# Performance work log

Hardware: AMD Instinct MI355X
Metric: run time of the kernel (lower is better)

Reference implementation:

```python
import jax, jax.numpy as jnp
import numpy as np

B, K, BIN = 16, 2048, 256
GRU, EMB, HID = 1024, 1024, 1024
H, KV = 16, 4
D = HID // H          # 64 head dim
NREP = H // KV        # 4 GQA repeat factor


def rotate_half(x):
    x1, x2 = jnp.split(x, 2, axis=-1)
    return jnp.concatenate((-x2, x1), axis=-1)


def setup_inputs() -> dict:
    key = jax.random.key(0)
    ks = jax.random.split(key, 8)
    h = jax.random.normal(ks[0], (B, K, GRU), dtype=jnp.float32)
    # real RoPE frequency tables, shape (BIN, D)
    inv_freq = 1.0 / (10000.0 ** (jnp.arange(0, D, 2, dtype=jnp.float32) / D))
    t = jnp.arange(BIN, dtype=jnp.float32)
    freqs = jnp.outer(t, inv_freq)                      # (BIN, D/2)
    emb = jnp.concatenate((freqs, freqs), axis=-1)      # (BIN, D)
    freqs_cos, freqs_sin = jnp.cos(emb), jnp.sin(emb)
    s = lambda fan: 1.0 / np.sqrt(fan).astype(np.float32)
    Wq = jax.random.normal(ks[1], (H * D, EMB), jnp.float32) * s(EMB)
    Wk = jax.random.normal(ks[2], (KV * D, GRU), jnp.float32) * s(GRU)
    Wv = jax.random.normal(ks[3], (KV * D, GRU), jnp.float32) * s(GRU)
    Wo = jax.random.normal(ks[4], (EMB, H * D), jnp.float32) * s(H * D)
    output_queries = jax.random.normal(ks[5], (BIN, EMB), jnp.float32)
    Wr = jax.random.normal(ks[6], (2, EMB), jnp.float32) * s(EMB)
    br = jnp.zeros((2,), jnp.float32)
    return {"h": h, "freqs_cos": freqs_cos, "freqs_sin": freqs_sin,
            "Wq": Wq, "Wk": Wk, "Wv": Wv, "Wo": Wo,
            "output_queries": output_queries, "Wr": Wr, "br": br}


def reference(h, freqs_cos, freqs_sin, Wq, Wk, Wv, Wo, output_queries, Wr, br):
    # KV projections from GRU history: (B, K, KV, D)
    k = (h @ Wk.T).reshape(B, K, KV, D)
    v = (h @ Wv.T).reshape(B, K, KV, D)
    # Queries are batch-invariant learned tokens: (BIN, H, D)
    q = (output_queries @ Wq.T).reshape(BIN, H, D)
    cos = freqs_cos[:, None, :]  # (BIN, 1, D) broadcast over heads
    sin = freqs_sin[:, None, :]
    q = q * cos + rotate_half(q) * sin
    # GQA: repeat_interleave KV heads to H heads
    k_rep = jnp.repeat(k, NREP, axis=2)  # (B, K, H, D)
    v_rep = jnp.repeat(v, NREP, axis=2)
    scores = jnp.einsum('qhd,bkhd->bhqk', q, k_rep) / np.sqrt(D).astype(np.float32)
    attn = jax.nn.softmax(scores, axis=-1)               # dropout p=0 (eval)
    out = jnp.einsum('bhqk,bkhd->bqhd', attn, v_rep).reshape(B, BIN, H * D)
    z = out @ Wo.T                                        # (B, BIN, EMB)
    return z @ Wr.T + br                                  # (B, BIN, 2)
```

## Files before the change

### kernel.cpp

```cpp
#include <hip/hip_runtime.h>

typedef __attribute__((ext_vector_type(8))) short short8;
typedef __attribute__((ext_vector_type(4))) float f32x4;
typedef __attribute__((ext_vector_type(16))) float f32x16;

#define DEV static __device__ __forceinline__

DEV unsigned short f2bf(float f) {
  unsigned int u = __float_as_uint(f);
  u += 0x7fff + ((u >> 16) & 1);
  return (unsigned short)(u >> 16);
}

DEV unsigned int cvtpk(float lo, float hi) {
  unsigned int r;
  asm("v_cvt_pk_bf16_f32 %0, %1, %2" : "=v"(r) : "v"(lo), "v"(hi));
  return r;
}

DEV f32x4 mfma16(short8 a, short8 b, f32x4 c) {
  return __builtin_amdgcn_mfma_f32_16x16x32_bf16(a, b, c, 0, 0, 0);
}

DEV f32x16 mfma32(short8 a, short8 b, f32x16 c) {
  return __builtin_amdgcn_mfma_f32_32x32x16_bf16(a, b, c, 0, 0, 0);
}

DEV void gl_lds16(const void* g, void* l) {
  __builtin_amdgcn_global_load_lds((const __attribute__((address_space(1))) void*)g,
                                   (__attribute__((address_space(3))) void*)l, 16, 0, 0);
}

__global__ __launch_bounds__(256) void cvtB_kernel(const float* __restrict__ Wq,
                                                   const float* __restrict__ Wk,
                                                   const float* __restrict__ Wv,
                                                   unsigned short* __restrict__ wqb,
                                                   unsigned short* __restrict__ wkvb) {
  int id = blockIdx.x * 256 + threadIdx.x;
  int e = id * 4;
  float4 v;
  unsigned short* d;
  if (e < 1048576)      { v = *(const float4*)(Wq + e);             d = wqb + e; }
  else if (e < 1310720) { v = *(const float4*)(Wk + (e - 1048576)); d = wkvb + (e - 1048576); }
  else                  { v = *(const float4*)(Wv + (e - 1310720)); d = wkvb + 262144 + (e - 1310720); }
  uint2 pk;
  pk.x = cvtpk(v.x, v.y);
  pk.y = cvtpk(v.z, v.w);
  *(uint2*)d = pk;
}

__global__ __launch_bounds__(256) void wrp_partial(const float* __restrict__ Wr,
                                                   const float* __restrict__ Wo,
                                                   float* __restrict__ part) {
  int blk = blockIdx.x;
  int tid = threadIdx.x;
  float a0[4] = {0.f,0.f,0.f,0.f};
  float a1[4] = {0.f,0.f,0.f,0.f};
  int e0 = blk * 64;
  for (int e = e0; e < e0 + 64; e++) {
    float w0 = Wr[e];
    float w1 = Wr[1024 + e];
    #pragma unroll
    for (int j4 = 0; j4 < 4; j4++) {
      float wo = Wo[(size_t)e * 1024 + j4 * 256 + tid];
      a0[j4] += w0 * wo;
      a1[j4] += w1 * wo;
    }
  }
  #pragma unroll
  for (int j4 = 0; j4 < 4; j4++) {
    part[blk * 2048 + 0    + j4 * 256 + tid] = a0[j4];
    part[blk * 2048 + 1024 + j4 * 256 + tid] = a1[j4];
  }
}

__global__ __launch_bounds__(256) void wrp_reduce(const float* __restrict__ part,
                                                  float* __restrict__ Wrp) {
  int id = blockIdx.x * 256 + threadIdx.x;
  float s = 0.f;
  #pragma unroll
  for (int blk = 0; blk < 16; blk++) s += part[blk * 2048 + id];
  Wrp[id] = s;
}

__global__ __launch_bounds__(512, 2) void gemm_kv(const float* __restrict__ A,
                                                  const unsigned short* __restrict__ Bb,
                                                  unsigned short* __restrict__ ok,
                                                  unsigned short* __restrict__ ov) {
  __shared__ float Asl[3][4096];
  __shared__ unsigned short Bsl[3][16384];

  int bid = blockIdx.x;
  int sw = (bid & 7) * 32 + (bid >> 3);
  int m0 = sw * 128;

  int tid = threadIdx.x;
  int w = tid >> 6, l = tid & 63;
  int l4 = l >> 4, l15 = l & 15;

  int ra = tid >> 3, ua = tid & 7;
  const float* gaA  = A + (size_t)(m0 + ra) * 1024 + ((ua ^ (ra & 7)) * 4);
  const float* gaA2 = gaA + (size_t)64 * 1024;
  const unsigned short* gbB = Bb + (size_t)(tid >> 2) * 1024
                                 + (((tid & 3) ^ ((tid >> 3) & 3)) * 8);

  int aoff0 = l15 * 128 + (((l4 * 2)     ^ (l15 & 7)) * 16);
  int aoff1 = l15 * 128 + (((l4 * 2 + 1) ^ (l15 & 7)) * 16);
  int boff = (w * 64 + l15) * 64 + ((l4 ^ ((l15 >> 1) & 3)) * 16);

  f32x4 acc[8][4];
  #pragma unroll
  for (int i = 0; i < 8; i++)
    #pragma unroll
    for (int j = 0; j < 4; j++) acc[i][j] = (f32x4)(0.f);

  #define STAGE(T, SB)                                                      \
    { const float* a0p = gaA  + (T) * 32;                                   \
      const float* a1p = gaA2 + (T) * 32;                                   \
      gl_lds16(a0p, (char*)Asl[SB] + tid * 16);                             \
      gl_lds16(a1p, (char*)Asl[SB] + 8192 + tid * 16);                      \
      const unsigned short* b0p = gbB + (T) * 32;                           \
      gl_lds16(b0p,          (char*)Bsl[SB] + tid * 16);                    \
      gl_lds16(b0p + 131072, (char*)Bsl[SB] + 8192  + tid * 16);            \
      gl_lds16(b0p + 262144, (char*)Bsl[SB] + 16384 + tid * 16);            \
      gl_lds16(b0p + 393216, (char*)Bsl[SB] + 24576 + tid * 16); }

  #define COMPUTE(CB)                                                       \
    { const char* Ab = (const char*)Asl[CB];                                \
      const char* Bf = (const char*)Bsl[CB];                                \
      short8 bfr[4];                                                        \
      _Pragma("unroll")                                                     \
      for (int j = 0; j < 4; j++)                                           \
        bfr[j] = *(const short8*)(Bf + boff + j * 1024);                    \
      _Pragma("unroll")                                                     \
      for (int i = 0; i < 8; i++) {                                         \
        float4 x = *(const float4*)(Ab + aoff0 + i * 2048);                 \
        float4 y = *(const float4*)(Ab + aoff1 + i * 2048);                 \
        union { short8 s; unsigned int u[4]; } af;                          \
        af.u[0] = cvtpk(x.x, x.y); af.u[1] = cvtpk(x.z, x.w);               \
        af.u[2] = cvtpk(y.x, y.y); af.u[3] = cvtpk(y.z, y.w);               \
        _Pragma("unroll")                                                   \
        for (int j = 0; j < 4; j++)                                         \
          acc[i][j] = mfma16(af.s, bfr[j], acc[i][j]);                      \
      } }

  #define WAIT6                                                             \
    { asm volatile("s_waitcnt vmcnt(6)" ::: "memory");                      \
      __builtin_amdgcn_s_barrier();                                         \
      __builtin_amdgcn_sched_barrier(0); }

  #define WAIT0                                                             \
    { asm volatile("s_waitcnt vmcnt(0)" ::: "memory");                      \
      __builtin_amdgcn_s_barrier();                                         \
      __builtin_amdgcn_sched_barrier(0); }

  STAGE(0, 0);
  STAGE(1, 1);
  asm volatile("s_waitcnt vmcnt(6)" ::: "memory");
  __builtin_amdgcn_s_barrier();
  __builtin_amdgcn_sched_barrier(0);

  #pragma unroll 1
  for (int tb = 0; tb < 30; tb += 3) {
    STAGE(tb + 2, 2); COMPUTE(0); WAIT6;
    STAGE(tb + 3, 0); COMPUTE(1); WAIT6;
    STAGE(tb + 4, 1); COMPUTE(2); WAIT6;
  }
  COMPUTE(0);
  WAIT0;
  COMPUTE(1);

  #undef STAGE
  #undef COMPUTE
  #undef WAIT6
  #undef WAIT0

  #pragma unroll
  for (int i = 0; i < 8; i++)
    #pragma unroll
    for (int j = 0; j < 4; j++) {
      int n = w * 64 + j * 16 + l15;
      int kvv = n >> 6, d = n & 63;
      #pragma unroll
      for (int r = 0; r < 4; r++) {
        int m = m0 + i * 16 + l4 * 4 + r;
        int bb = m >> 11, kk = m & 2047;
        unsigned short val = f2bf(acc[i][j][r]);
        if (kvv < 4)
          ok[((size_t)(bb * 4 + kvv) * 2048 + kk) * 64 + d] = val;
        else
          ov[((size_t)(bb * 4 + (kvv - 4)) * 64 + d) * 2048 + kk] = val;
      }
    }
}

__global__ __launch_bounds__(256) void gemm_q(const float* __restrict__ A,
                                              const unsigned short* __restrict__ Bb,
                                              float* __restrict__ of) {
  __shared__ unsigned short Asm[2][4096];
  __shared__ unsigned short Bsm[2][4096];

  int bid = blockIdx.x;
  int ksplit = bid >> 4;
  int m0 = ((bid >> 3) & 1) * 128;
  int n0 = (bid & 7) * 128;
  int t0 = ksplit * 8;
  constexpr int nt = 8;

  int tid = threadIdx.x;
  int w = tid >> 6, l = tid & 63;
  int l4 = l >> 4, l15 = l & 15;
  int wm = w >> 1, wn = w & 1;

  int ra = w * 32 + (l >> 1);
  int rx = (l >> 2) & 3;
  const float* ga = A + (size_t)(m0 + ra) * 1024 + t0 * 32 + (l & 1) * 16;
  int pw0 = (2 * (l & 1) + 0) ^ rx;
  int pw1 = (2 * (l & 1) + 1) ^ rx;
  int awb0 = ra * 64 + pw0 * 16;
  int awb1 = ra * 64 + pw1 * 16;

  int rb = w * 32 + (l >> 2);
  int cb = ((l & 3) ^ ((l >> 3) & 3)) * 8;
  const unsigned short* gb = Bb + (size_t)(n0 + rb) * 1024 + t0 * 32 + cb;

  int qsw = l4 ^ ((l15 >> 1) & 3);
  int arb = (wm * 64 + l15) * 64 + qsw * 16;
  int brb = (wn * 64 + l15) * 64 + qsw * 16;

  f32x4 acc[4][4];
  #pragma unroll
  for (int i = 0; i < 4; i++)
    #pragma unroll
    for (int j = 0; j < 4; j++) acc[i][j] = (f32x4)(0.f);

  float4 fa0, fa1, fa2, fa3;

  #define LOADA(tt)                                                        \
    { const float* gA = ga + (tt) * 32;                                    \
      fa0 = *(const float4*)(gA);                                          \
      fa1 = *(const float4*)(gA + 4);                                      \
      fa2 = *(const float4*)(gA + 8);                                      \
      fa3 = *(const float4*)(gA + 12); }

  #define WRITEA(bufi)                                                     \
    { union { short8 s; unsigned int u[4]; } t0u, t1u;                     \
      t0u.u[0] = cvtpk(fa0.x, fa0.y); t0u.u[1] = cvtpk(fa0.z, fa0.w);      \
      t0u.u[2] = cvtpk(fa1.x, fa1.y); t0u.u[3] = cvtpk(fa1.z, fa1.w);      \
      t1u.u[0] = cvtpk(fa2.x, fa2.y); t1u.u[1] = cvtpk(fa2.z, fa2.w);      \
      t1u.u[2] = cvtpk(fa3.x, fa3.y); t1u.u[3] = cvtpk(fa3.z, fa3.w);      \
      *(short8*)((char*)Asm[bufi] + awb0) = t0u.s;                         \
      *(short8*)((char*)Asm[bufi] + awb1) = t1u.s; }

  #define STAGEB(bufi, tt)                                                 \
    { char* lb = (char*)Bsm[bufi] + w * 2048;                              \
      const unsigned short* gB = gb + (tt) * 32;                           \
      gl_lds16(gB, lb);                                                    \
      gl_lds16(gB + 16384, lb + 1024); }

  LOADA(0);
  STAGEB(0, 0);
  WRITEA(0);
  __syncthreads();

  for (int t = 0; t < nt; t++) {
    int buf = t & 1;
    if (t + 1 < nt) {
      LOADA(t + 1);
      STAGEB(buf ^ 1, t + 1);
    }
    short8 af[4], bfg[4];
    #pragma unroll
    for (int i = 0; i < 4; i++)
      af[i] = *(const short8*)((char*)Asm[buf] + arb + i * 1024);
    #pragma unroll
    for (int j = 0; j < 4; j++)
      bfg[j] = *(const short8*)((char*)Bsm[buf] + brb + j * 1024);
    #pragma unroll
    for (int i = 0; i < 4; i++)
      #pragma unroll
      for (int j = 0; j < 4; j++)
        acc[i][j] = mfma16(af[i], bfg[j], acc[i][j]);
    if (t + 1 < nt) WRITEA(buf ^ 1);
    __syncthreads();
  }
  #undef LOADA
  #undef WRITEA
  #undef STAGEB

  float* o = of + (size_t)ksplit * 262144;
  #pragma unroll
  for (int i = 0; i < 4; i++)
    #pragma unroll
    for (int j = 0; j < 4; j++) {
      int n = n0 + wn * 64 + j * 16 + l15;
      #pragma unroll
      for (int r = 0; r < 4; r++) {
        int m = m0 + wm * 64 + i * 16 + l4 * 4 + r;
        o[(size_t)m * 1024 + n] = acc[i][j][r];
      }
    }
}

__global__ __launch_bounds__(256) void rope_kernel(const float* __restrict__ qp,
                                                   const float* __restrict__ cosb,
                                                   const float* __restrict__ sinb,
                                                   unsigned short* __restrict__ qb) {
  int id = blockIdx.x * 256 + threadIdx.x;
  int qrow = id >> 10, hd = id & 1023, hh = hd >> 6, d = hd & 63;
  int od = hh * 64 + ((d < 32) ? d + 32 : d - 32);
  float v = 0.f, o = 0.f;
  #pragma unroll
  for (int s4 = 0; s4 < 4; s4++) {
    v += qp[s4 * 262144 + qrow * 1024 + hd];
    o += qp[s4 * 262144 + qrow * 1024 + od];
  }
  if (d < 32) o = -o;
  float c = cosb[qrow * 64 + d];
  float s = sinb[qrow * 64 + d];
  float outv = (v * c + o * s) * 0.18033688011112042f;
  qb[((size_t)hh * 256 + qrow) * 64 + d] = f2bf(outv);
}

__global__ __launch_bounds__(256) void attn_kernel(const unsigned short* __restrict__ qb,
                                                   const unsigned short* __restrict__ kb,
                                                   const unsigned short* __restrict__ vb,
                                                   const float* __restrict__ Wrp,
                                                   float* __restrict__ part) {
  __shared__ unsigned short Kt[2][2048];
  __shared__ unsigned short Vt[2][2048];

  int bid = blockIdx.x;
  int x = bid & 7, mid = (bid >> 3) & 7, top = bid >> 6;
  int g = mid * 8 + x;
  int b = g >> 2, kvh = g & 3;
  int hl = top >> 1, qh = top & 1;
  int h = kvh * 4 + hl;

  int tid = threadIdx.x;
  int w = tid >> 6, l = tid & 63;
  int q31 = l & 31, L = l >> 5;
  int qg = qh * 128 + w * 32 + q31;

  const unsigned short* kg = kb + (size_t)(b * 4 + kvh) * 2048 * 64;
  const unsigned short* vg = vb + (size_t)(b * 4 + kvh) * 64 * 2048;

  short8 qf[4];
  #pragma unroll
  for (int c = 0; c < 4; c++)
    qf[c] = *(const short8*)&qb[((size_t)h * 256 + qg) * 64 + c * 16 + L * 8];

  f32x16 Ot[2];
  Ot[0] = (f32x16)(0.f); Ot[1] = (f32x16)(0.f);
  float m = -1e30f, lsum = 0.f;

  int ksrow = tid >> 3, kslot = tid & 7;
  const unsigned short* ksrc = kg + (size_t)ksrow * 64 + ((kslot ^ (ksrow & 7)) * 8);
  int vsrow = tid >> 2, vslot = tid & 3;
  const unsigned short* vsrc = vg + (size_t)vsrow * 2048 + ((vslot ^ (vsrow & 3)) * 8);

  #define STAGE(bufi, tt)                                                    \
    { gl_lds16(ksrc + (size_t)(tt) * 2048, (char*)Kt[bufi] + tid * 16);      \
      gl_lds16(vsrc + (tt) * 32,           (char*)Vt[bufi] + tid * 16); }

  STAGE(0, 0);
  __syncthreads();

  for (int t = 0; t < 64; t++) {
    int buf = t & 1;
    if (t + 1 < 64) STAGE(buf ^ 1, t + 1);

    f32x16 st = (f32x16)(0.f);
    #pragma unroll
    for (int c = 0; c < 4; c++) {
      int row = q31;
      int byt = row * 128 + (((c * 2 + L) ^ (row & 7)) * 16);
      short8 kf = *(const short8*)((char*)Kt[buf] + byt);
      st = mfma32(kf, qf[c], st);
    }

    float mx = fmaxf(fmaxf(fmaxf(st[0], st[1]), fmaxf(st[2], st[3])),
                     fmaxf(fmaxf(st[4], st[5]), fmaxf(st[6], st[7])));
    float mx2 = fmaxf(fmaxf(fmaxf(st[8], st[9]), fmaxf(st[10], st[11])),
                      fmaxf(fmaxf(st[12], st[13]), fmaxf(st[14], st[15])));
    mx = fmaxf(mx, mx2);
    mx = fmaxf(mx, __shfl_xor(mx, 32));

    if (!__all(mx <= m + 8.f)) {
      float mnew = fmaxf(m, mx);
      float corr = exp2f(m - mnew);
      lsum *= corr;
      #pragma unroll
      for (int db = 0; db < 2; db++)
        #pragma unroll
        for (int r = 0; r < 16; r++) Ot[db][r] *= corr;
      m = mnew;
    }

    float p[16];
    float ls = 0.f;
    #pragma unroll
    for (int r = 0; r < 16; r++) {
      p[r] = exp2f(st[r] - m);
      ls += p[r];
    }
    lsum += ls;

    unsigned int pw[2][4];
    #pragma unroll
    for (int kc = 0; kc < 2; kc++) {
      unsigned int A0 = cvtpk(p[kc * 8 + 0], p[kc * 8 + 1]);
      unsigned int A1 = cvtpk(p[kc * 8 + 2], p[kc * 8 + 3]);
      unsigned int B0 = cvtpk(p[kc * 8 + 4], p[kc * 8 + 5]);
      unsigned int B1 = cvtpk(p[kc * 8 + 6], p[kc * 8 + 7]);
      asm volatile("v_permlane32_swap_b32 %0, %1" : "+v"(A0), "+v"(B0));
      asm volatile("v_permlane32_swap_b32 %0, %1" : "+v"(A1), "+v"(B1));
      pw[kc][0] = A0; pw[kc][1] = A1; pw[kc][2] = B0; pw[kc][3] = B1;
    }

    #pragma unroll
    for (int db = 0; db < 2; db++) {
      int drow = db * 32 + q31;
      #pragma unroll
      for (int kc = 0; kc < 2; kc++) {
        int byt = drow * 64 + (((kc * 2 + L) ^ (drow & 3)) * 16);
        short8 vf = *(const short8*)((char*)Vt[buf] + byt);
        short8 pf;
        {
          union { short8 s; unsigned int u[4]; } uu;
          uu.u[0] = pw[kc][0]; uu.u[1] = pw[kc][1];
          uu.u[2] = pw[kc][2]; uu.u[3] = pw[kc][3];
          pf = uu.s;
        }
        Ot[db] = mfma32(vf, pf, Ot[db]);
      }
    }

    __syncthreads();
  }
  #undef STAGE

  lsum += __shfl_xor(lsum, 32);
  float rinv = 1.0f / lsum;

  float a0 = 0.f, a1 = 0.f;
  #pragma unroll
  for (int db = 0; db < 2; db++)
    #pragma unroll
    for (int rq = 0; rq < 4; rq++) {
      int dbase = db * 32 + rq * 8 + L * 4;
      float4 w0v = *(const float4*)(Wrp + h * 64 + dbase);
      float4 w1v = *(const float4*)(Wrp + 1024 + h * 64 + dbase);
      #pragma unroll
      for (int j = 0; j < 4; j++) {
        float o = Ot[db][rq * 4 + j] * rinv;
        a0 += o * ((const float*)&w0v)[j];
        a1 += o * ((const float*)&w1v)[j];
      }
    }
  a0 += __shfl_xor(a0, 32);
  a1 += __shfl_xor(a1, 32);

  if (L == 0) {
    size_t base = ((size_t)(b * 16 + h) * 256 + qg) * 2;
    float2 r2; r2.x = a0; r2.y = a1;
    *(float2*)&part[base] = r2;
  }
}

__global__ __launch_bounds__(256) void final_kernel(const float* __restrict__ part,
                                                    const float* __restrict__ br,
                                                    float* __restrict__ out) {
  int id = blockIdx.x * 256 + threadIdx.x;
  int c = id & 1, q = (id >> 1) & 255, b = id >> 9;
  float s = br[c];
  #pragma unroll
  for (int hh = 0; hh < 16; hh++)
    s += part[(((size_t)(b * 16 + hh) * 256) + q) * 2 + c];
  out[id] = s;
}

extern "C" void kernel_launch(void* const* d_in, const int* in_sizes, int n_in,
                              void* d_out, int out_size, void* d_ws, size_t ws_size,
                              hipStream_t stream) {
  const float* h    = (const float*)d_in[0];
  const float* fcos = (const float*)d_in[1];
  const float* fsin = (const float*)d_in[2];
  const float* Wq   = (const float*)d_in[3];
  const float* Wk   = (const float*)d_in[4];
  const float* Wv   = (const float*)d_in[5];
  const float* Wo   = (const float*)d_in[6];
  const float* oq   = (const float*)d_in[7];
  const float* Wr   = (const float*)d_in[8];
  const float* br   = (const float*)d_in[9];
  float* out = (float*)d_out;

  char* ws = (char*)d_ws;
  unsigned short* kbuf = (unsigned short*)(ws);
  unsigned short* vbuf = (unsigned short*)(ws + 16777216);
  float* qpart         = (float*)(ws + 33554432);
  unsigned short* qbf  = (unsigned short*)(ws + 37748736);
  float* wpart         = (float*)(ws + 38273024);
  float* Wrp           = (float*)(ws + 38404096);
  float* apart         = (float*)(ws + 38412288);
  unsigned short* wqb  = (unsigned short*)(ws + 38936576);
  unsigned short* wkvb = (unsigned short*)(ws + 41033728);

  cvtB_kernel<<<dim3(1536), dim3(256), 0, stream>>>(Wq, Wk, Wv, wqb, wkvb);
  wrp_partial<<<dim3(16), dim3(256), 0, stream>>>(Wr, Wo, wpart);
  wrp_reduce<<<dim3(8), dim3(256), 0, stream>>>(wpart, Wrp);
  gemm_q<<<dim3(64), dim3(256), 0, stream>>>(oq, wqb, qpart);
  rope_kernel<<<dim3(1024), dim3(256), 0, stream>>>(qpart, fcos, fsin, qbf);
  gemm_kv<<<dim3(256), dim3(512), 0, stream>>>(h, wkvb, kbuf, vbuf);
  attn_kernel<<<dim3(512), dim3(256), 0, stream>>>(qbf, kbuf, vbuf, Wrp, apart);
  final_kernel<<<dim3(32), dim3(256), 0, stream>>>(apart, br, out);
}
```

Measured before the change: 167.8 us.

## Split attention over KV halves and pre-convert A tiles to bf16 in GEMM

```diff
diff --git a/kernel.cpp b/kernel.cpp
--- a/kernel.cpp
+++ b/kernel.cpp
@@ -15,6 +15,12 @@
 DEV unsigned int cvtpk(float lo, float hi) {
   unsigned int r;
   asm("v_cvt_pk_bf16_f32 %0, %1, %2" : "=v"(r) : "v"(lo), "v"(hi));
+  return r;
+}
+
+DEV float max3f(float a, float b, float c) {
+  float r;
+  asm("v_max3_f32 %0, %1, %2, %3" : "=v"(r) : "v"(a), "v"(b), "v"(c));
   return r;
 }
 
@@ -87,7 +93,7 @@
                                                   const unsigned short* __restrict__ Bb,
                                                   unsigned short* __restrict__ ok,
                                                   unsigned short* __restrict__ ov) {
-  __shared__ float Asl[3][4096];
+  __shared__ unsigned short Asl[3][4096];
   __shared__ unsigned short Bsl[3][16384];
 
   int bid = blockIdx.x;
@@ -98,15 +104,16 @@
   int w = tid >> 6, l = tid & 63;
   int l4 = l >> 4, l15 = l & 15;
 
-  int ra = tid >> 3, ua = tid & 7;
-  const float* gaA  = A + (size_t)(m0 + ra) * 1024 + ((ua ^ (ra & 7)) * 4);
-  const float* gaA2 = gaA + (size_t)64 * 1024;
+  int arow = tid >> 2, ac = tid & 3;
+  const float* ga = A + (size_t)(m0 + arow) * 1024 + ac * 8;
+  int awb = arow * 64 + ((ac ^ ((arow >> 1) & 3)) * 16);
+
   const unsigned short* gbB = Bb + (size_t)(tid >> 2) * 1024
                                  + (((tid & 3) ^ ((tid >> 3) & 3)) * 8);
 
-  int aoff0 = l15 * 128 + (((l4 * 2)     ^ (l15 & 7)) * 16);
-  int aoff1 = l15 * 128 + (((l4 * 2 + 1) ^ (l15 & 7)) * 16);
-  int boff = (w * 64 + l15) * 64 + ((l4 ^ ((l15 >> 1) & 3)) * 16);
+  int fsw = (l4 ^ ((l15 >> 1) & 3)) * 16;
+  int aoff = l15 * 64 + fsw;
+  int boff = (w * 64 + l15) * 64 + fsw;
 
   f32x4 acc[8][4];
   #pragma unroll
@@ -114,16 +121,25 @@
     #pragma unroll
     for (int j = 0; j < 4; j++) acc[i][j] = (f32x4)(0.f);
 
-  #define STAGE(T, SB)                                                      \
-    { const float* a0p = gaA  + (T) * 32;                                   \
-      const float* a1p = gaA2 + (T) * 32;                                   \
-      gl_lds16(a0p, (char*)Asl[SB] + tid * 16);                             \
-      gl_lds16(a1p, (char*)Asl[SB] + 8192 + tid * 16);                      \
-      const unsigned short* b0p = gbB + (T) * 32;                           \
+  float4 aXx, aXy, aYx, aYy;
+
+  #define LOADA(T, RX, RY)                                                  \
+    { const float* gA = ga + (T) * 32;                                      \
+      RX = *(const float4*)(gA);                                            \
+      RY = *(const float4*)(gA + 4); }
+
+  #define STAGEB(SB, T)                                                     \
+    { const unsigned short* b0p = gbB + (T) * 32;                           \
       gl_lds16(b0p,          (char*)Bsl[SB] + tid * 16);                    \
       gl_lds16(b0p + 131072, (char*)Bsl[SB] + 8192  + tid * 16);            \
       gl_lds16(b0p + 262144, (char*)Bsl[SB] + 16384 + tid * 16);            \
       gl_lds16(b0p + 393216, (char*)Bsl[SB] + 24576 + tid * 16); }
+
+  #define WRITEA(WB, RX, RY)                                                \
+    { union { short8 s; unsigned int u[4]; } af;                            \
+      af.u[0] = cvtpk(RX.x, RX.y); af.u[1] = cvtpk(RX.z, RX.w);             \
+      af.u[2] = cvtpk(RY.x, RY.y); af.u[3] = cvtpk(RY.z, RY.w);             \
+      *(short8*)((char*)Asl[WB] + awb) = af.s; }
 
   #define COMPUTE(CB)                                                       \
     { const char* Ab = (const char*)Asl[CB];                                \
@@ -132,48 +148,63 @@
       _Pragma("unroll")                                                     \
       for (int j = 0; j < 4; j++)                                           \
         bfr[j] = *(const short8*)(Bf + boff + j * 1024);                    \
+      __builtin_amdgcn_s_setprio(1);                                        \
       _Pragma("unroll")                                                     \
       for (int i = 0; i < 8; i++) {                                         \
-        float4 x = *(const float4*)(Ab + aoff0 + i * 2048);                 \
-        float4 y = *(const float4*)(Ab + aoff1 + i * 2048);                 \
-        union { short8 s; unsigned int u[4]; } af;                          \
-        af.u[0] = cvtpk(x.x, x.y); af.u[1] = cvtpk(x.z, x.w);               \
-        af.u[2] = cvtpk(y.x, y.y); af.u[3] = cvtpk(y.z, y.w);               \
+        short8 af = *(const short8*)(Ab + aoff + i * 1024);                 \
         _Pragma("unroll")                                                   \
         for (int j = 0; j < 4; j++)                                         \
-          acc[i][j] = mfma16(af.s, bfr[j], acc[i][j]);                      \
-      } }
-
-  #define WAIT6                                                             \
+          acc[i][j] = mfma16(af, bfr[j], acc[i][j]);                        \
+      }                                                                     \
+      __builtin_amdgcn_s_setprio(0); }
+
+  #define ENDSTEP                                                           \
     { asm volatile("s_waitcnt vmcnt(6)" ::: "memory");                      \
+      asm volatile("s_waitcnt lgkmcnt(0)" ::: "memory");                    \
       __builtin_amdgcn_s_barrier();                                         \
       __builtin_amdgcn_sched_barrier(0); }
 
-  #define WAIT0                                                             \
-    { asm volatile("s_waitcnt vmcnt(0)" ::: "memory");                      \
-      __builtin_amdgcn_s_barrier();                                         \
-      __builtin_amdgcn_sched_barrier(0); }
-
-  STAGE(0, 0);
-  STAGE(1, 1);
+  LOADA(0, aXx, aXy);
+  STAGEB(0, 0);
+  WRITEA(0, aXx, aXy);
+  LOADA(1, aXx, aXy);
+  STAGEB(1, 1);
   asm volatile("s_waitcnt vmcnt(6)" ::: "memory");
+  asm volatile("s_waitcnt lgkmcnt(0)" ::: "memory");
   __builtin_amdgcn_s_barrier();
   __builtin_amdgcn_sched_barrier(0);
 
+  #define STEPE(T, CB, WB, SB)               \
+    { LOADA((T) + 2, aYx, aYy); STAGEB(SB, (T) + 2);                        \
+      COMPUTE(CB); WRITEA(WB, aXx, aXy); ENDSTEP }
+  #define STEPO(T, CB, WB, SB)                \
+    { LOADA((T) + 2, aXx, aXy); STAGEB(SB, (T) + 2);                        \
+      COMPUTE(CB); WRITEA(WB, aYx, aYy); ENDSTEP }
+
   #pragma unroll 1
-  for (int tb = 0; tb < 30; tb += 3) {
-    STAGE(tb + 2, 2); COMPUTE(0); WAIT6;
-    STAGE(tb + 3, 0); COMPUTE(1); WAIT6;
-    STAGE(tb + 4, 1); COMPUTE(2); WAIT6;
+  for (int tb = 0; tb < 30; tb += 6) {
+    STEPE(tb + 0, 0, 1, 2);
+    STEPO(tb + 1, 1, 2, 0);
+    STEPE(tb + 2, 2, 0, 1);
+    STEPO(tb + 3, 0, 1, 2);
+    STEPE(tb + 4, 1, 2, 0);
+    STEPO(tb + 5, 2, 0, 1);
   }
   COMPUTE(0);
-  WAIT0;
+  WRITEA(1, aXx, aXy);
+  asm volatile("s_waitcnt vmcnt(0)" ::: "memory");
+  asm volatile("s_waitcnt lgkmcnt(0)" ::: "memory");
+  __builtin_amdgcn_s_barrier();
+  __builtin_amdgcn_sched_barrier(0);
   COMPUTE(1);
 
-  #undef STAGE
+  #undef LOADA
+  #undef STAGEB
+  #undef WRITEA
   #undef COMPUTE
-  #undef WAIT6
-  #undef WAIT0
+  #undef ENDSTEP
+  #undef STEPE
+  #undef STEPO
 
   #pragma unroll
   for (int i = 0; i < 8; i++)
@@ -331,9 +362,11 @@
   __shared__ unsigned short Vt[2][2048];
 
   int bid = blockIdx.x;
-  int x = bid & 7, mid = (bid >> 3) & 7, top = bid >> 6;
+  int x = bid & 7, mid = (bid >> 3) & 7, top2 = bid >> 6;
   int g = mid * 8 + x;
   int b = g >> 2, kvh = g & 3;
+  int split = top2 >> 3;
+  int top = top2 & 7;
   int hl = top >> 1, qh = top & 1;
   int h = kvh * 4 + hl;
 
@@ -359,16 +392,18 @@
   int vsrow = tid >> 2, vslot = tid & 3;
   const unsigned short* vsrc = vg + (size_t)vsrow * 2048 + ((vslot ^ (vsrow & 3)) * 8);
 
+  int tb0 = split * 32;
+
   #define STAGE(bufi, tt)                                                    \
     { gl_lds16(ksrc + (size_t)(tt) * 2048, (char*)Kt[bufi] + tid * 16);      \
       gl_lds16(vsrc + (tt) * 32,           (char*)Vt[bufi] + tid * 16); }
 
-  STAGE(0, 0);
+  STAGE(0, tb0);
   __syncthreads();
 
-  for (int t = 0; t < 64; t++) {
+  for (int t = 0; t < 32; t++) {
     int buf = t & 1;
-    if (t + 1 < 64) STAGE(buf ^ 1, t + 1);
+    if (t + 1 < 32) STAGE(buf ^ 1, tb0 + t + 1);
 
     f32x16 st = (f32x16)(0.f);
     #pragma unroll
@@ -379,11 +414,12 @@
       st = mfma32(kf, qf[c], st);
     }
 
-    float mx = fmaxf(fmaxf(fmaxf(st[0], st[1]), fmaxf(st[2], st[3])),
-                     fmaxf(fmaxf(st[4], st[5]), fmaxf(st[6], st[7])));
-    float mx2 = fmaxf(fmaxf(fmaxf(st[8], st[9]), fmaxf(st[10], st[11])),
-                      fmaxf(fmaxf(st[12], st[13]), fmaxf(st[14], st[15])));
-    mx = fmaxf(mx, mx2);
+    float g0 = max3f(st[0], st[1], st[2]);
+    float g1 = max3f(st[3], st[4], st[5]);
+    float g2 = max3f(st[6], st[7], st[8]);
+    float g3 = max3f(st[9], st[10], st[11]);
+    float g4 = max3f(st[12], st[13], st[14]);
+    float mx = fmaxf(max3f(g0, g1, g2), max3f(g3, g4, st[15]));
     mx = fmaxf(mx, __shfl_xor(mx, 32));
 
     if (!__all(mx <= m + 8.f)) {
@@ -441,7 +477,6 @@
   #undef STAGE
 
   lsum += __shfl_xor(lsum, 32);
-  float rinv = 1.0f / lsum;
 
   float a0 = 0.f, a1 = 0.f;
   #pragma unroll
@@ -453,7 +488,7 @@
       float4 w1v = *(const float4*)(Wrp + 1024 + h * 64 + dbase);
       #pragma unroll
       for (int j = 0; j < 4; j++) {
-        float o = Ot[db][rq * 4 + j] * rinv;
+        float o = Ot[db][rq * 4 + j];
         a0 += o * ((const float*)&w0v)[j];
         a1 += o * ((const float*)&w1v)[j];
       }
@@ -462,9 +497,10 @@
   a1 += __shfl_xor(a1, 32);
 
   if (L == 0) {
-    size_t base = ((size_t)(b * 16 + h) * 256 + qg) * 2;
-    float2 r2; r2.x = a0; r2.y = a1;
-    *(float2*)&part[base] = r2;
+    size_t base = ((((size_t)(b * 16 + h) * 256 + qg) * 2) + split) * 4;
+    float4 r4;
+    r4.x = m; r4.y = lsum; r4.z = a0; r4.w = a1;
+    *(float4*)&part[base] = r4;
   }
 }
 
@@ -475,8 +511,16 @@
   int c = id & 1, q = (id >> 1) & 255, b = id >> 9;
   float s = br[c];
   #pragma unroll
-  for (int hh = 0; hh < 16; hh++)
-    s += part[(((size_t)(b * 16 + hh) * 256) + q) * 2 + c];
+  for (int hh = 0; hh < 16; hh++) {
+    size_t base = (((size_t)(b * 16 + hh) * 256 + q) * 2) * 4;
+    float4 f0 = *(const float4*)&part[base];
+    float4 f1 = *(const float4*)&part[base + 4];
+    float mm = fmaxf(f0.x, f1.x);
+    float w0 = exp2f(f0.x - mm), w1 = exp2f(f1.x - mm);
+    float den = w0 * f0.y + w1 * f1.y;
+    float num = (c == 0) ? (w0 * f0.z + w1 * f1.z) : (w0 * f0.w + w1 * f1.w);
+    s += num / den;
+  }
   out[id] = s;
 }
 
@@ -503,8 +547,8 @@
   float* wpart         = (float*)(ws + 38273024);
   float* Wrp           = (float*)(ws + 38404096);
   float* apart         = (float*)(ws + 38412288);
-  unsigned short* wqb  = (unsigned short*)(ws + 38936576);
-  unsigned short* wkvb = (unsigned short*)(ws + 41033728);
+  unsigned short* wqb  = (unsigned short*)(ws + 40509440);
+  unsigned short* wkvb = (unsigned short*)(ws + 42606592);
 
   cvtB_kernel<<<dim3(1536), dim3(256), 0, stream>>>(Wq, Wk, Wv, wqb, wkvb);
   wrp_partial<<<dim3(16), dim3(256), 0, stream>>>(Wr, Wo, wpart);
@@ -512,6 +556,6 @@
   gemm_q<<<dim3(64), dim3(256), 0, stream>>>(oq, wqb, qpart);
   rope_kernel<<<dim3(1024), dim3(256), 0, stream>>>(qpart, fcos, fsin, qbf);
   gemm_kv<<<dim3(256), dim3(512), 0, stream>>>(h, wkvb, kbuf, vbuf);
-  attn_kernel<<<dim3(512), dim3(256), 0, stream>>>(qbf, kbuf, vbuf, Wrp, apart);
+  attn_kernel<<<dim3(1024), dim3(256), 0, stream>>>(qbf, kbuf, vbuf, Wrp, apart);
   final_kernel<<<dim3(32), dim3(256), 0, stream>>>(apart, br, out);
 }
```

New measurement: 161.0 us. -4.1%, faster.
